# Optimization experiments

Measured on AMD Instinct MI355X. Metric: run time of the kernel, lower is better.

Reference implementation:

```python
import jax, jax.numpy as jnp
import numpy as np

N_NODES = 50000
N_EDGES = 800000
N_GRAPHS = 64
F_IN = 128
HID = 64
HEADS = 4
N_CLS = 10
NEG_SLOPE = 0.2


def _glorot(key, shape):
    fan_in, fan_out = shape[-1], shape[-2] if len(shape) > 1 else shape[-1]
    lim = jnp.sqrt(6.0 / (fan_in + fan_out))
    return jax.random.uniform(key, shape, jnp.float32, -lim, lim)


def setup_inputs() -> dict:
    key = jax.random.key(0)
    ks = jax.random.split(key, 20)
    x = jax.random.normal(ks[0], (N_NODES, F_IN), jnp.float32)
    edge_index = jax.random.randint(ks[1], (2, N_EDGES), 0, N_NODES, jnp.int32)
    batch = jnp.sort(jax.random.randint(ks[2], (N_NODES,), 0, N_GRAPHS, jnp.int32))
    HC = HID * HEADS
    return {
        "x": x, "edge_index": edge_index, "batch": batch,
        # node embedding Linear(F_IN -> HID)
        "W_emb": _glorot(ks[3], (HID, F_IN)), "b_emb": jnp.zeros((HID,), jnp.float32),
        # gat1: HID -> HID, heads=4, concat
        "W1": _glorot(ks[4], (HC, HID)),
        "a_src1": _glorot(ks[5], (HEADS, HID)), "a_dst1": _glorot(ks[6], (HEADS, HID)),
        "b1": jnp.zeros((HC,), jnp.float32),
        # gat2: HC -> HID, heads=4, concat
        "W2": _glorot(ks[7], (HC, HC)),
        "a_src2": _glorot(ks[8], (HEADS, HID)), "a_dst2": _glorot(ks[9], (HEADS, HID)),
        "b2": jnp.zeros((HC,), jnp.float32),
        # gat3: HC -> HID, heads=1, mean
        "W3": _glorot(ks[10], (HID, HC)),
        "a_src3": _glorot(ks[11], (1, HID)), "a_dst3": _glorot(ks[12], (1, HID)),
        "b3": jnp.zeros((HID,), jnp.float32),
        # classifier: Linear(2*HID -> HID), ReLU, Linear(HID -> N_CLS)
        "Wc1": _glorot(ks[13], (HID, 2 * HID)), "bc1": jnp.zeros((HID,), jnp.float32),
        "Wc2": _glorot(ks[14], (N_CLS, HID)), "bc2": jnp.zeros((N_CLS,), jnp.float32),
    }


def _gat_layer(x, src, dst, W, a_src, a_dst, b, concat):
    """PyG-style GATConv (eval mode, self-loops already in src/dst)."""
    N = x.shape[0]
    H, C = a_src.shape
    h = (x @ W.T).reshape(N, H, C)                       # [N,H,C]
    s = jnp.einsum("nhc,hc->nh", h, a_src)               # [N,H]
    d = jnp.einsum("nhc,hc->nh", h, a_dst)               # [N,H]
    e = jax.nn.leaky_relu(s[src] + d[dst], NEG_SLOPE)    # [E,H]
    emax = jax.lax.stop_gradient(jax.ops.segment_max(e, dst, num_segments=N))
    emax = jnp.where(jnp.isfinite(emax), emax, 0.0)
    ex = jnp.exp(e - emax[dst])
    den = jax.ops.segment_sum(ex, dst, num_segments=N)   # [N,H]
    alpha = ex / (den[dst] + 1e-16)                      # segment softmax
    out = jax.ops.segment_sum(h[src] * alpha[:, :, None], dst, num_segments=N)
    out = out.reshape(N, H * C) if concat else out.mean(axis=1)
    return out + b


def reference(x, edge_index, batch, W_emb, b_emb, W1, a_src1, a_dst1, b1,
              W2, a_src2, a_dst2, b2, W3, a_src3, a_dst3, b3, Wc1, bc1, Wc2, bc2):
    N = x.shape[0]
    loops = jnp.arange(N, dtype=edge_index.dtype)
    src = jnp.concatenate([edge_index[0], loops])
    dst = jnp.concatenate([edge_index[1], loops])

    h = x @ W_emb.T + b_emb
    h = jax.nn.elu(_gat_layer(h, src, dst, W1, a_src1, a_dst1, b1, True))
    h = jax.nn.elu(_gat_layer(h, src, dst, W2, a_src2, a_dst2, b2, True))
    h = jax.nn.elu(_gat_layer(h, src, dst, W3, a_src3, a_dst3, b3, False))

    counts = jax.ops.segment_sum(jnp.ones((N,), h.dtype), batch, num_segments=N_GRAPHS)
    mean = jax.ops.segment_sum(h, batch, num_segments=N_GRAPHS) / jnp.maximum(counts, 1.0)[:, None]
    mx = jax.ops.segment_max(h, batch, num_segments=N_GRAPHS)
    mx = jnp.where(counts[:, None] > 0, mx, 0.0)
    g = jnp.concatenate([mean, mx], axis=1)              # [B, 2*HID]

    g = jax.nn.relu(g @ Wc1.T + bc1)
    return g @ Wc2.T + bc2                               # [B, N_CLS]
```

## Files before the change

kernel.cpp:

```cpp
#include <hip/hip_runtime.h>
#include <math.h>

#define NG 64
#define F_IN 128
#define NEG_SLOPE 0.2f

typedef __attribute__((ext_vector_type(8))) short s16x8;
typedef __attribute__((ext_vector_type(4))) float f32x4;

static __device__ __forceinline__ float elu_f(float x) { return x > 0.f ? x : expm1f(x); }
static __device__ __forceinline__ float lrelu(float x) { return x > 0.f ? x : NEG_SLOPE * x; }
static __device__ __forceinline__ unsigned enc_f32(float x) {
    unsigned u = __float_as_uint(x);
    return (u & 0x80000000u) ? ~u : (u | 0x80000000u);
}
static __device__ __forceinline__ float dec_f32(unsigned u) {
    unsigned b = (u & 0x80000000u) ? (u & 0x7fffffffu) : ~u;
    return __uint_as_float(b);
}
static __device__ __forceinline__ unsigned short bf16_rn(float x) {
    unsigned u = __float_as_uint(x);
    unsigned r = u + 0x7FFFu + ((u >> 16) & 1u);
    return (unsigned short)(r >> 16);
}
static __device__ __forceinline__ float bf16_to_f32(unsigned short h) {
    return __uint_as_float(((unsigned)h) << 16);
}

static __device__ __forceinline__ size_t fragaddr(int row, int k, int K) {
    return ((size_t)(row >> 4) * (K >> 5) + (k >> 5)) * 512
         + (size_t)(((k & 31) >> 3) * 128 + (row & 15) * 8 + (k & 7));
}

static __device__ __forceinline__ void frag_store8(const float* v, unsigned short* hi,
                                                   unsigned short* lo, int row, int k0, int K) {
    unsigned short h[8], l[8];
    #pragma unroll
    for (int i = 0; i < 8; ++i) {
        h[i] = bf16_rn(v[i]);
        l[i] = bf16_rn(v[i] - bf16_to_f32(h[i]));
    }
    size_t a = fragaddr(row, k0, K);
    *(ushort4*)&hi[a]     = make_ushort4(h[0], h[1], h[2], h[3]);
    *(ushort4*)&hi[a + 4] = make_ushort4(h[4], h[5], h[6], h[7]);
    *(ushort4*)&lo[a]     = make_ushort4(l[0], l[1], l[2], l[3]);
    *(ushort4*)&lo[a + 4] = make_ushort4(l[4], l[5], l[6], l[7]);
}

__global__ void convert_frag(const float* __restrict__ in, unsigned short* __restrict__ hi,
                             unsigned short* __restrict__ lo, int R, int K) {
    int t = blockIdx.x * blockDim.x + threadIdx.x;
    if (t * 8 >= R * K) return;
    int row = (t * 8) / K;
    int k0 = (t * 8) % K;
    float4 v0 = *(const float4*)&in[(size_t)row * K + k0];
    float4 v1 = *(const float4*)&in[(size_t)row * K + k0 + 4];
    float v[8] = {v0.x, v0.y, v0.z, v0.w, v1.x, v1.y, v1.z, v1.w};
    frag_store8(v, hi, lo, row, k0, K);
}

__global__ void convert_weights(const float* __restrict__ We, const float* __restrict__ W1,
                                const float* __restrict__ W2, const float* __restrict__ W3,
                                unsigned short* WhE, unsigned short* WlE,
                                unsigned short* Wh1, unsigned short* Wl1,
                                unsigned short* Wh2, unsigned short* Wl2,
                                unsigned short* Wh3, unsigned short* Wl3) {
    int b = blockIdx.x;
    const float* in; unsigned short* hi; unsigned short* lo; int R, K, base;
    if (b < 4)       { in = We; hi = WhE; lo = WlE; R = 64;  K = 128; base = 0; }
    else if (b < 12) { in = W1; hi = Wh1; lo = Wl1; R = 256; K = 64;  base = 4; }
    else if (b < 44) { in = W2; hi = Wh2; lo = Wl2; R = 256; K = 256; base = 12; }
    else             { in = W3; hi = Wh3; lo = Wl3; R = 64;  K = 256; base = 44; }
    int t = (b - base) * 256 + threadIdx.x;
    if (t * 8 >= R * K) return;
    int row = (t * 8) / K;
    int k0 = (t * 8) % K;
    float4 v0 = *(const float4*)&in[(size_t)row * K + k0];
    float4 v1 = *(const float4*)&in[(size_t)row * K + k0 + 4];
    float v[8] = {v0.x, v0.y, v0.z, v0.w, v1.x, v1.y, v1.z, v1.w};
    frag_store8(v, hi, lo, row, k0, K);
}

__global__ void uvec_kernel(const float* __restrict__ W1, const float* __restrict__ a1s,
                            const float* __restrict__ a1d,
                            float* __restrict__ us, float* __restrict__ ud) {
    int h = threadIdx.x >> 6;
    int i = threadIdx.x & 63;
    float s = 0.f, d = 0.f;
    for (int o = 0; o < 64; ++o) {
        float w = W1[(h * 64 + o) * 64 + i];
        s = fmaf(w, a1s[h * 64 + o], s);
        d = fmaf(w, a1d[h * 64 + o], d);
    }
    us[h * 64 + i] = s;
    ud[h * 64 + i] = d;
}

__global__ void hist_kernel(const int* __restrict__ ei, int* __restrict__ cnt, int E, int N) {
    int e = blockIdx.x * blockDim.x + threadIdx.x;
    int ET = E + N;
    if (e >= ET) return;
    int dst = (e < E) ? ei[E + e] : (e - E);
    atomicAdd(&cnt[dst], 1);
}

__global__ void scan1_kernel(const int* __restrict__ cnt, int* __restrict__ excl,
                             int* __restrict__ bsum, int n) {
    __shared__ int sm[256];
    int t = threadIdx.x;
    int base = blockIdx.x * 1024 + t * 4;
    int v[4];
    #pragma unroll
    for (int u = 0; u < 4; ++u) { int idx = base + u; v[u] = (idx < n) ? cnt[idx] : 0; }
    int tsum = v[0] + v[1] + v[2] + v[3];
    sm[t] = tsum;
    __syncthreads();
    for (int off = 1; off < 256; off <<= 1) {
        int y = (t >= off) ? sm[t - off] : 0;
        __syncthreads();
        sm[t] += y;
        __syncthreads();
    }
    int run = sm[t] - tsum;
    #pragma unroll
    for (int u = 0; u < 4; ++u) {
        int idx = base + u;
        if (idx < n) excl[idx] = run;
        run += v[u];
    }
    if (t == 255) bsum[blockIdx.x] = sm[255];
}

__global__ void scan2_kernel(int* __restrict__ bsum, int* __restrict__ offs, int nb, int n) {
    if (blockIdx.x == 0 && threadIdx.x == 0) {
        int run = 0;
        for (int b = 0; b < nb; ++b) { int t = bsum[b]; bsum[b] = run; run += t; }
        offs[n] = run;
    }
}

__global__ void scan3_kernel(int* __restrict__ offs, const int* __restrict__ bsum,
                             int* __restrict__ cur, int n) {
    int base = blockIdx.x * 1024 + threadIdx.x * 4;
    int add = bsum[blockIdx.x];
    #pragma unroll
    for (int u = 0; u < 4; ++u) {
        int idx = base + u;
        if (idx < n) { int v = offs[idx] + add; offs[idx] = v; cur[idx] = v; }
    }
}

__global__ void scatter_kernel(const int* __restrict__ ei, int* __restrict__ cur,
                               int* __restrict__ csr_src, int E, int N) {
    int e = blockIdx.x * blockDim.x + threadIdx.x;
    int ET = E + N;
    if (e >= ET) return;
    int src, dst;
    if (e < E) { src = ei[e]; dst = ei[E + e]; }
    else       { src = e - E; dst = e - E; }
    int pos = atomicAdd(&cur[dst], 1);
    csr_src[pos] = src;
}

template<int K, int AK, int BN, int HATT, bool SHARED, bool SLICED, bool DO_ELU, int OUTM>
__global__ __launch_bounds__(256) void gemm_frag(const unsigned short* __restrict__ Ahi,
                                                 const unsigned short* __restrict__ Alo,
                                                 const unsigned short* __restrict__ Whi,
                                                 const unsigned short* __restrict__ Wlo,
                                                 void* __restrict__ OutV,
                                                 unsigned short* __restrict__ Ohi,
                                                 unsigned short* __restrict__ Olo,
                                                 int M,
                                                 const float* __restrict__ bias,
                                                 const float* __restrict__ asrc,
                                                 const float* __restrict__ adst,
                                                 float* __restrict__ S, float* __restrict__ D,
                                                 int N) {
    constexpr int RF = (BN == 256) ? 4 : 2;
    const int t = threadIdx.x;
    const int lane = t & 63;
    const int w = t >> 6;
    const int lj = lane & 15;
    const int kg = lane >> 4;
    const int n0 = blockIdx.x * ((BN == 256) ? 64 : 128);
    const int m0 = blockIdx.y * BN;
    const int rbase = (BN == 256) ? 0 : w * 32;
    const int cbase = (BN == 256) ? w * 64 : 0;
    const int aoff = SLICED ? blockIdx.y * K : 0;
    const unsigned short* __restrict__ WhiB = SLICED ? Whi + (size_t)blockIdx.y * BN * K : Whi;
    const unsigned short* __restrict__ WloB = SLICED ? Wlo + (size_t)blockIdx.y * BN * K : Wlo;

    f32x4 acc[RF][4];
    #pragma unroll
    for (int rf = 0; rf < RF; ++rf)
        #pragma unroll
        for (int cf = 0; cf < 4; ++cf) acc[rf][cf] = (f32x4){0.f, 0.f, 0.f, 0.f};

    for (int kc = 0; kc < K; kc += 32) {
        s16x8 ah[RF], al[RF];
        #pragma unroll
        for (int rf = 0; rf < RF; ++rf) {
            size_t a = fragaddr(n0 + rbase + rf * 16 + lj, aoff + kc + kg * 8, AK);
            ah[rf] = *(const s16x8*)&Ahi[a];
            al[rf] = *(const s16x8*)&Alo[a];
        }
        #pragma unroll
        for (int cf = 0; cf < 4; ++cf) {
            int bcol = (SLICED ? 0 : m0) + cbase + cf * 16 + lj;
            size_t b = fragaddr(bcol, kc + kg * 8, K);
            s16x8 bh = *(const s16x8*)&WhiB[b];
            s16x8 bl = *(const s16x8*)&WloB[b];
            #pragma unroll
            for (int rf = 0; rf < RF; ++rf) {
                acc[rf][cf] = __builtin_amdgcn_mfma_f32_16x16x32_bf16(ah[rf], bh, acc[rf][cf], 0, 0, 0);
                acc[rf][cf] = __builtin_amdgcn_mfma_f32_16x16x32_bf16(ah[rf], bl, acc[rf][cf], 0, 0, 0);
                acc[rf][cf] = __builtin_amdgcn_mfma_f32_16x16x32_bf16(al[rf], bh, acc[rf][cf], 0, 0, 0);
            }
        }
    }

    #pragma unroll
    for (int cf = 0; cf < 4; ++cf) {
        int gcol = m0 + cbase + cf * 16 + lj;
        float bv = bias ? bias[gcol] : 0.f;
        #pragma unroll
        for (int rf = 0; rf < RF; ++rf) {
            #pragma unroll
            for (int r = 0; r < 4; ++r) {
                int gn = n0 + rbase + rf * 16 + (lane >> 4) * 4 + r;
                if (gn < N) {
                    float o = acc[rf][cf][r] + bv;
                    if (DO_ELU) o = elu_f(o);
                    if (OUTM == 0) {
                        ((float*)OutV)[(size_t)gn * M + gcol] = o;
                    } else if (OUTM == 1) {
                        ((unsigned short*)OutV)[(size_t)gn * M + gcol] = bf16_rn(o);
                    } else {
                        unsigned short hv = bf16_rn(o);
                        unsigned short lv = bf16_rn(o - bf16_to_f32(hv));
                        size_t a2 = fragaddr(gn, gcol, M);
                        Ohi[a2] = hv; Olo[a2] = lv;
                    }
                }
            }
        }
    }
    if (HATT > 0) {
        const int HS = SHARED ? HATT : 1;
        #pragma unroll
        for (int hh = 0; hh < HS; ++hh) {
            const int head = SHARED ? hh : w;
            float aw[4], dw[4], bw[4];
            #pragma unroll
            for (int c2 = 0; c2 < 4; ++c2) {
                aw[c2] = asrc[head * 64 + c2 * 16 + lj];
                dw[c2] = adst[head * 64 + c2 * 16 + lj];
                bw[c2] = bias ? bias[m0 + cbase + c2 * 16 + lj] : 0.f;
            }
            #pragma unroll
            for (int rf = 0; rf < RF; ++rf) {
                #pragma unroll
                for (int r = 0; r < 4; ++r) {
                    float sp = 0.f, dp = 0.f;
                    #pragma unroll
                    for (int c2 = 0; c2 < 4; ++c2) {
                        float vv = acc[rf][c2][r] + bw[c2];
                        sp = fmaf(vv, aw[c2], sp);
                        dp = fmaf(vv, dw[c2], dp);
                    }
                    #pragma unroll
                    for (int off = 1; off < 16; off <<= 1) {
                        sp += __shfl_xor(sp, off);
                        dp += __shfl_xor(dp, off);
                    }
                    if (lj == 0) {
                        int gn = n0 + rbase + rf * 16 + (lane >> 4) * 4 + r;
                        if (gn < N) { S[gn * HATT + head] = sp; D[gn * HATT + head] = dp; }
                    }
                }
            }
        }
    }
}

__global__ __launch_bounds__(256, 8) void gat_agg_x(const unsigned short* __restrict__ xb,
                                                    const float* __restrict__ s,
                                                    const float* __restrict__ d,
                                                    const int* __restrict__ offs,
                                                    const int* __restrict__ csr_src,
                                                    unsigned short* __restrict__ Gh,
                                                    unsigned short* __restrict__ Gl,
                                                    int N) {
    __shared__ float stash[4][64 * 5];
    int wv = threadIdx.x >> 6;
    int lane = threadIdx.x & 63;
    int node = (blockIdx.x * blockDim.x + threadIdx.x) >> 6;
    if (node >= N) return;
    float* st = stash[wv];
    int e0 = offs[node], e1 = offs[node + 1];
    float4 dv4 = *(const float4*)&d[node * 4];
    float dd[4] = {dv4.x, dv4.y, dv4.z, dv4.w};
    float mrun[4] = {-INFINITY, -INFINITY, -INFINITY, -INFINITY};
    float den[4] = {0.f, 0.f, 0.f, 0.f};
    float acc[4] = {0.f, 0.f, 0.f, 0.f};

    for (int base = e0; base < e1; base += 64) {
        int cnt = min(64, e1 - base);
        float ev[4] = {-INFINITY, -INFINITY, -INFINITY, -INFINITY};
        if (lane < cnt) {
            int src = csr_src[base + lane];
            float4 sv = *(const float4*)&s[src * 4];
            ev[0] = lrelu(sv.x + dd[0]); ev[1] = lrelu(sv.y + dd[1]);
            ev[2] = lrelu(sv.z + dd[2]); ev[3] = lrelu(sv.w + dd[3]);
            st[lane * 5 + 0] = ev[0]; st[lane * 5 + 1] = ev[1];
            st[lane * 5 + 2] = ev[2]; st[lane * 5 + 3] = ev[3];
            st[lane * 5 + 4] = __int_as_float(src);
        }
        #pragma unroll
        for (int h = 0; h < 4; ++h) {
            float m = ev[h];
            #pragma unroll
            for (int off = 32; off; off >>= 1) m = fmaxf(m, __shfl_xor(m, off));
            float mnew = fmaxf(mrun[h], m);
            float scale = __expf(mrun[h] - mnew);
            acc[h] *= scale; den[h] *= scale;
            mrun[h] = mnew;
        }
        int k = 0;
        for (; k + 4 <= cnt; k += 4) {
            int si[4];
            #pragma unroll
            for (int u = 0; u < 4; ++u) si[u] = __float_as_int(st[(k + u) * 5 + 4]);
            float vx[4];
            #pragma unroll
            for (int u = 0; u < 4; ++u) vx[u] = bf16_to_f32(xb[(size_t)si[u] * 64 + lane]);
            #pragma unroll
            for (int u = 0; u < 4; ++u) {
                #pragma unroll
                for (int h = 0; h < 4; ++h) {
                    float p = __expf(st[(k + u) * 5 + h] - mrun[h]);
                    den[h] += p;
                    acc[h] = fmaf(p, vx[u], acc[h]);
                }
            }
        }
        for (; k < cnt; ++k) {
            int src = __float_as_int(st[k * 5 + 4]);
            float v = bf16_to_f32(xb[(size_t)src * 64 + lane]);
            #pragma unroll
            for (int h = 0; h < 4; ++h) {
                float p = __expf(st[k * 5 + h] - mrun[h]);
                den[h] += p;
                acc[h] = fmaf(p, v, acc[h]);
            }
        }
    }
    #pragma unroll
    for (int h = 0; h < 4; ++h) {
        float v = acc[h] / (den[h] + 1e-16f);
        unsigned short hv = bf16_rn(v);
        unsigned short lv = bf16_rn(v - bf16_to_f32(hv));
        size_t a = fragaddr(node, h * 64 + lane, 256);
        Gh[a] = hv; Gl[a] = lv;
    }
}

template<bool FRAGOUT>
__global__ __launch_bounds__(256, 8) void gat_agg4(const unsigned short* __restrict__ hp,
                                                   const float* __restrict__ s,
                                                   const float* __restrict__ d,
                                                   const int* __restrict__ offs,
                                                   const int* __restrict__ csr_src,
                                                   const float* __restrict__ bias,
                                                   float* __restrict__ outF,
                                                   unsigned short* __restrict__ outHi,
                                                   unsigned short* __restrict__ outLo,
                                                   int N) {
    __shared__ float stash[4][64 * 5];
    int wv = threadIdx.x >> 6;
    int lane = threadIdx.x & 63;
    int node = (blockIdx.x * blockDim.x + threadIdx.x) >> 6;
    if (node >= N) return;
    float* st = stash[wv];
    int e0 = offs[node], e1 = offs[node + 1];

    float4 dv4 = *(const float4*)&d[node * 4];
    float dd[4] = {dv4.x, dv4.y, dv4.z, dv4.w};
    const int hd = lane >> 4;

    float mrun = -INFINITY;
    float acc0 = 0.f, acc1 = 0.f, acc2 = 0.f, acc3 = 0.f, den = 0.f;

    for (int base = e0; base < e1; base += 64) {
        int cnt = min(64, e1 - base);
        float ev[4] = {-INFINITY, -INFINITY, -INFINITY, -INFINITY};
        if (lane < cnt) {
            int src = csr_src[base + lane];
            float4 sv = *(const float4*)&s[src * 4];
            ev[0] = lrelu(sv.x + dd[0]); ev[1] = lrelu(sv.y + dd[1]);
            ev[2] = lrelu(sv.z + dd[2]); ev[3] = lrelu(sv.w + dd[3]);
            st[lane * 5 + 0] = ev[0]; st[lane * 5 + 1] = ev[1];
            st[lane * 5 + 2] = ev[2]; st[lane * 5 + 3] = ev[3];
            st[lane * 5 + 4] = __int_as_float(src);
        }
        float mc[4];
        #pragma unroll
        for (int h = 0; h < 4; ++h) {
            float m = ev[h];
            #pragma unroll
            for (int off = 32; off; off >>= 1) m = fmaxf(m, __shfl_xor(m, off));
            mc[h] = m;
        }
        float mch = (lane & 32) ? ((lane & 16) ? mc[3] : mc[2]) : ((lane & 16) ? mc[1] : mc[0]);
        float mnew = fmaxf(mrun, mch);
        float scale = __expf(mrun - mnew);
        acc0 *= scale; acc1 *= scale; acc2 *= scale; acc3 *= scale; den *= scale;
        mrun = mnew;

        int k = 0;
        for (; k + 4 <= cnt; k += 4) {
            float ea = st[(k + 0) * 5 + hd];
            float eb = st[(k + 1) * 5 + hd];
            float ec = st[(k + 2) * 5 + hd];
            float ed = st[(k + 3) * 5 + hd];
            int sa = __float_as_int(st[(k + 0) * 5 + 4]);
            int sb = __float_as_int(st[(k + 1) * 5 + 4]);
            int sc = __float_as_int(st[(k + 2) * 5 + 4]);
            int sd_ = __float_as_int(st[(k + 3) * 5 + 4]);
            float pa = __expf(ea - mrun);
            float pb = __expf(eb - mrun);
            float pc = __expf(ec - mrun);
            float pd = __expf(ed - mrun);
            den += (pa + pb) + (pc + pd);
            uint2 ua = *(const uint2*)&hp[(size_t)sa * 256 + lane * 4];
            uint2 ub = *(const uint2*)&hp[(size_t)sb * 256 + lane * 4];
            uint2 uc = *(const uint2*)&hp[(size_t)sc * 256 + lane * 4];
            uint2 ud = *(const uint2*)&hp[(size_t)sd_ * 256 + lane * 4];
            acc0 = fmaf(pa, __uint_as_float((ua.x & 0xffffu) << 16), acc0);
            acc1 = fmaf(pa, __uint_as_float(ua.x & 0xffff0000u), acc1);
            acc2 = fmaf(pa, __uint_as_float((ua.y & 0xffffu) << 16), acc2);
            acc3 = fmaf(pa, __uint_as_float(ua.y & 0xffff0000u), acc3);
            acc0 = fmaf(pb, __uint_as_float((ub.x & 0xffffu) << 16), acc0);
            acc1 = fmaf(pb, __uint_as_float(ub.x & 0xffff0000u), acc1);
            acc2 = fmaf(pb, __uint_as_float((ub.y & 0xffffu) << 16), acc2);
            acc3 = fmaf(pb, __uint_as_float(ub.y & 0xffff0000u), acc3);
            acc0 = fmaf(pc, __uint_as_float((uc.x & 0xffffu) << 16), acc0);
            acc1 = fmaf(pc, __uint_as_float(uc.x & 0xffff0000u), acc1);
            acc2 = fmaf(pc, __uint_as_float((uc.y & 0xffffu) << 16), acc2);
            acc3 = fmaf(pc, __uint_as_float(uc.y & 0xffff0000u), acc3);
            acc0 = fmaf(pd, __uint_as_float((ud.x & 0xffffu) << 16), acc0);
            acc1 = fmaf(pd, __uint_as_float(ud.x & 0xffff0000u), acc1);
            acc2 = fmaf(pd, __uint_as_float((ud.y & 0xffffu) << 16), acc2);
            acc3 = fmaf(pd, __uint_as_float(ud.y & 0xffff0000u), acc3);
        }
        for (; k < cnt; ++k) {
            float e = st[k * 5 + hd];
            int src = __float_as_int(st[k * 5 + 4]);
            float p = __expf(e - mrun);
            den += p;
            uint2 uv = *(const uint2*)&hp[(size_t)src * 256 + lane * 4];
            acc0 = fmaf(p, __uint_as_float((uv.x & 0xffffu) << 16), acc0);
            acc1 = fmaf(p, __uint_as_float(uv.x & 0xffff0000u), acc1);
            acc2 = fmaf(p, __uint_as_float((uv.y & 0xffffu) << 16), acc2);
            acc3 = fmaf(p, __uint_as_float(uv.y & 0xffff0000u), acc3);
        }
    }

    float inv = 1.0f / (den + 1e-16f);
    float4 bv = *(const float4*)&bias[lane * 4];
    float o0 = elu_f(acc0 * inv + bv.x);
    float o1 = elu_f(acc1 * inv + bv.y);
    float o2 = elu_f(acc2 * inv + bv.z);
    float o3 = elu_f(acc3 * inv + bv.w);
    if (FRAGOUT) {
        unsigned short h0 = bf16_rn(o0), h1 = bf16_rn(o1), h2 = bf16_rn(o2), h3 = bf16_rn(o3);
        ushort4 hq = make_ushort4(h0, h1, h2, h3);
        ushort4 lq = make_ushort4(bf16_rn(o0 - bf16_to_f32(h0)),
                                  bf16_rn(o1 - bf16_to_f32(h1)),
                                  bf16_rn(o2 - bf16_to_f32(h2)),
                                  bf16_rn(o3 - bf16_to_f32(h3)));
        size_t a = fragaddr(node, lane * 4, 256);
        *(ushort4*)&outHi[a] = hq;
        *(ushort4*)&outLo[a] = lq;
    } else {
        float4 o = make_float4(o0, o1, o2, o3);
        *(float4*)&outF[(size_t)node * 256 + lane * 4] = o;
    }
}

__global__ __launch_bounds__(256, 8) void gat_agg1(const unsigned short* __restrict__ hp,
                                                   const float* __restrict__ s,
                                                   const float* __restrict__ d,
                                                   const int* __restrict__ offs,
                                                   const int* __restrict__ csr_src,
                                                   const float* __restrict__ bias,
                                                   float* __restrict__ outF, int N) {
    __shared__ float stash[4][64 * 2];
    int wv = threadIdx.x >> 6;
    int lane = threadIdx.x & 63;
    int node = (blockIdx.x * blockDim.x + threadIdx.x) >> 6;
    if (node >= N) return;
    float* st = stash[wv];
    int e0 = offs[node], e1 = offs[node + 1];
    float dd = d[node];

    float mrun = -INFINITY;
    float acc0 = 0.f, den = 0.f;

    for (int base = e0; base < e1; base += 64) {
        int cnt = min(64, e1 - base);
        float ev = -INFINITY;
        if (lane < cnt) {
            int src = csr_src[base + lane];
            ev = lrelu(s[src] + dd);
            st[lane * 2 + 0] = ev;
            st[lane * 2 + 1] = __int_as_float(src);
        }
        float m = ev;
        #pragma unroll
        for (int off = 32; off; off >>= 1) m = fmaxf(m, __shfl_xor(m, off));
        float mnew = fmaxf(mrun, m);
        float scale = __expf(mrun - mnew);
        acc0 *= scale; den *= scale;
        mrun = mnew;

        int k = 0;
        for (; k + 4 <= cnt; k += 4) {
            float ea = st[(k + 0) * 2];
            float eb = st[(k + 1) * 2];
            float ec = st[(k + 2) * 2];
            float ed = st[(k + 3) * 2];
            int sa = __float_as_int(st[(k + 0) * 2 + 1]);
            int sb = __float_as_int(st[(k + 1) * 2 + 1]);
            int sc = __float_as_int(st[(k + 2) * 2 + 1]);
            int sd_ = __float_as_int(st[(k + 3) * 2 + 1]);
            float pa = __expf(ea - mrun);
            float pb = __expf(eb - mrun);
            float pc = __expf(ec - mrun);
            float pd = __expf(ed - mrun);
            den += (pa + pb) + (pc + pd);
            float ha = bf16_to_f32(hp[(size_t)sa * 64 + lane]);
            float hb = bf16_to_f32(hp[(size_t)sb * 64 + lane]);
            float hc = bf16_to_f32(hp[(size_t)sc * 64 + lane]);
            float hdv = bf16_to_f32(hp[(size_t)sd_ * 64 + lane]);
            acc0 = fmaf(pa, ha, acc0);
            acc0 = fmaf(pb, hb, acc0);
            acc0 = fmaf(pc, hc, acc0);
            acc0 = fmaf(pd, hdv, acc0);
        }
        for (; k < cnt; ++k) {
            float e = st[k * 2];
            int src = __float_as_int(st[k * 2 + 1]);
            float p = __expf(e - mrun);
            den += p;
            acc0 = fmaf(p, bf16_to_f32(hp[(size_t)src * 64 + lane]), acc0);
        }
    }
    float inv = 1.0f / (den + 1e-16f);
    outF[(size_t)node * 64 + lane] = elu_f(acc0 * inv + bias[lane]);
}

__global__ void pool_init(float* gsum, unsigned* gmax, int* gcnt) {
    int t = blockIdx.x * blockDim.x + threadIdx.x;
    if (t < NG * 64) { gsum[t] = 0.f; gmax[t] = enc_f32(-INFINITY); }
    if (t < NG) gcnt[t] = 0;
}

__global__ void pool_reduce(const float* __restrict__ h3, const int* __restrict__ batch,
                            float* __restrict__ gsum, unsigned* __restrict__ gmax,
                            int* __restrict__ gcnt, int N, int per) {
    int w = (blockIdx.x * blockDim.x + threadIdx.x) >> 6;
    int lane = threadIdx.x & 63;
    int n0 = w * per;
    int n1 = min(N, n0 + per);
    float lsum = 0.f, lmax = -INFINITY;
    int cur = -1, cnt = 0;
    for (int n = n0; n < n1; ++n) {
        int g = batch[n];
        if (g != cur) {
            if (cur >= 0) {
                atomicAdd(&gsum[cur * 64 + lane], lsum);
                atomicMax(&gmax[cur * 64 + lane], enc_f32(lmax));
                if (lane == 0) atomicAdd(&gcnt[cur], cnt);
            }
            cur = g; lsum = 0.f; lmax = -INFINITY; cnt = 0;
        }
        float v = h3[(size_t)n * 64 + lane];
        lsum += v; lmax = fmaxf(lmax, v); cnt++;
    }
    if (cur >= 0) {
        atomicAdd(&gsum[cur * 64 + lane], lsum);
        atomicMax(&gmax[cur * 64 + lane], enc_f32(lmax));
        if (lane == 0) atomicAdd(&gcnt[cur], cnt);
    }
}

__global__ __launch_bounds__(128) void classifier(const float* __restrict__ gsum,
                                                  const unsigned* __restrict__ gmax,
                                                  const int* __restrict__ gcnt,
                                                  const float* __restrict__ Wc1,
                                                  const float* __restrict__ bc1,
                                                  const float* __restrict__ Wc2,
                                                  const float* __restrict__ bc2,
                                                  float* __restrict__ out) {
    __shared__ float gv[128];
    __shared__ float z1[64];
    int g = blockIdx.x, t = threadIdx.x;
    int cnt = gcnt[g];
    if (t < 64) {
        gv[t] = gsum[g * 64 + t] / fmaxf((float)cnt, 1.f);
    } else {
        float mx = dec_f32(gmax[g * 64 + (t - 64)]);
        gv[t] = (cnt > 0) ? mx : 0.f;
    }
    __syncthreads();
    if (t < 64) {
        float a = bc1[t];
        for (int k = 0; k < 128; ++k) a = fmaf(Wc1[t * 128 + k], gv[k], a);
        z1[t] = a > 0.f ? a : 0.f;
    }
    __syncthreads();
    if (t < 10) {
        float a = bc2[t];
        for (int k = 0; k < 64; ++k) a = fmaf(Wc2[t * 64 + k], z1[k], a);
        out[g * 10 + t] = a;
    }
}

extern "C" void kernel_launch(void* const* d_in, const int* in_sizes, int n_in,
                              void* d_out, int out_size, void* d_ws, size_t ws_size,
                              hipStream_t stream) {
    const float* x      = (const float*)d_in[0];
    const int*   ei     = (const int*)d_in[1];
    const int*   batch  = (const int*)d_in[2];
    const float* W_emb  = (const float*)d_in[3];
    const float* b_emb  = (const float*)d_in[4];
    const float* W1     = (const float*)d_in[5];
    const float* as1    = (const float*)d_in[6];
    const float* ad1    = (const float*)d_in[7];
    const float* b1     = (const float*)d_in[8];
    const float* W2     = (const float*)d_in[9];
    const float* as2    = (const float*)d_in[10];
    const float* ad2    = (const float*)d_in[11];
    const float* b2     = (const float*)d_in[12];
    const float* W3     = (const float*)d_in[13];
    const float* as3    = (const float*)d_in[14];
    const float* ad3    = (const float*)d_in[15];
    const float* b3     = (const float*)d_in[16];
    const float* Wc1    = (const float*)d_in[17];
    const float* bc1    = (const float*)d_in[18];
    const float* Wc2    = (const float*)d_in[19];
    const float* bc2    = (const float*)d_in[20];

    const int N = in_sizes[0] / F_IN;
    const int E = in_sizes[1] / 2;
    const int ET = E + N;
    const int GB64 = (N + 63) / 64;
    const int GB128 = (N + 127) / 128;
    const int ROWS_FR = ((N + 255) / 256) * 256;
    const size_t FR128 = (size_t)(ROWS_FR / 16) * (128 / 32) * 512;
    const size_t FR256 = (size_t)(ROWS_FR / 16) * (256 / 32) * 512;

    size_t off = 0;
    auto alloc = [&](size_t bytes) -> void* {
        void* p = (char*)d_ws + off;
        off += (bytes + 255) & ~(size_t)255;
        return p;
    };
    unsigned short* Xh  = (unsigned short*)alloc(FR128 * 2);
    unsigned short* Xl  = (unsigned short*)alloc(FR128 * 2);
    unsigned short* Aemb= (unsigned short*)alloc((size_t)N * 64 * 2);
    unsigned short* Gh  = (unsigned short*)alloc(FR256 * 2);
    unsigned short* Gl  = (unsigned short*)alloc(FR256 * 2);
    unsigned short* C1h = (unsigned short*)alloc(FR256 * 2);
    unsigned short* C1l = (unsigned short*)alloc(FR256 * 2);
    unsigned short* H2b = (unsigned short*)alloc((size_t)N * 256 * 2);
    unsigned short* WhE = (unsigned short*)alloc(64 * 128 * 2);
    unsigned short* WlE = (unsigned short*)alloc(64 * 128 * 2);
    unsigned short* Wh1 = (unsigned short*)alloc(256 * 64 * 2);
    unsigned short* Wl1 = (unsigned short*)alloc(256 * 64 * 2);
    unsigned short* Wh2 = (unsigned short*)alloc(256 * 256 * 2);
    unsigned short* Wl2 = (unsigned short*)alloc(256 * 256 * 2);
    unsigned short* Wh3 = (unsigned short*)alloc(64 * 256 * 2);
    unsigned short* Wl3 = (unsigned short*)alloc(64 * 256 * 2);
    float*    us1     = (float*)alloc(4 * 64 * 4);
    float*    ud1     = (float*)alloc(4 * 64 * 4);
    float*    S       = (float*)alloc((size_t)N * 4 * 4);
    float*    D       = (float*)alloc((size_t)N * 4 * 4);
    int*      offs    = (int*)alloc((size_t)(N + 1) * 4);
    int*      cnt     = (int*)alloc((size_t)N * 4);
    int*      bsum    = (int*)alloc(64 * 4);
    int*      csr_src = (int*)alloc((size_t)ET * 4);
    float*    gsum    = (float*)alloc(NG * 64 * 4);
    unsigned* gmax    = (unsigned*)alloc(NG * 64 * 4);
    int*      gcnt    = (int*)alloc(NG * 4);
    (void)ws_size; (void)n_in; (void)out_size;

    const int SCB = (N + 1023) / 1024;

    convert_frag<<<(N * 128 / 8 + 255) / 256, 256, 0, stream>>>(x, Xh, Xl, N, 128);
    convert_weights<<<52, 256, 0, stream>>>(W_emb, W1, W2, W3, WhE, WlE, Wh1, Wl1,
                                            Wh2, Wl2, Wh3, Wl3);
    uvec_kernel<<<1, 256, 0, stream>>>(W1, as1, ad1, us1, ud1);

    hipMemsetAsync(cnt, 0, (size_t)N * 4, stream);
    hist_kernel<<<(ET + 255) / 256, 256, 0, stream>>>(ei, cnt, E, N);
    scan1_kernel<<<SCB, 256, 0, stream>>>(cnt, offs, bsum, N);
    scan2_kernel<<<1, 64, 0, stream>>>(bsum, offs, SCB, N);
    scan3_kernel<<<SCB, 256, 0, stream>>>(offs, bsum, cnt, N);
    scatter_kernel<<<(ET + 255) / 256, 256, 0, stream>>>(ei, cnt, csr_src, E, N);

    const int NWV = (N * 64 + 255) / 256;

    gemm_frag<128, 128, 64, 4, true, false, false, 1><<<dim3(GB128, 1), 256, 0, stream>>>(
        Xh, Xl, WhE, WlE, Aemb, nullptr, nullptr, 64, b_emb, us1, ud1, S, D, N);
    gat_agg_x<<<NWV, 256, 0, stream>>>(Aemb, S, D, offs, csr_src, Gh, Gl, N);
    gemm_frag<64, 256, 64, 0, false, true, true, 3><<<dim3(GB128, 4), 256, 0, stream>>>(
        Gh, Gl, Wh1, Wl1, nullptr, C1h, C1l, 256, b1, nullptr, nullptr, nullptr, nullptr, N);
    gemm_frag<256, 256, 256, 4, false, false, false, 1><<<dim3(GB64, 1), 256, 0, stream>>>(
        C1h, C1l, Wh2, Wl2, H2b, nullptr, nullptr, 256, nullptr, as2, ad2, S, D, N);
    gat_agg4<true><<<NWV, 256, 0, stream>>>(H2b, S, D, offs, csr_src, b2,
                                            nullptr, Gh, Gl, N);
    gemm_frag<256, 256, 64, 1, true, false, false, 1><<<dim3(GB128, 1), 256, 0, stream>>>(
        Gh, Gl, Wh3, Wl3, Aemb, nullptr, nullptr, 64, nullptr, as3, ad3, S, D, N);
    gat_agg1<<<NWV, 256, 0, stream>>>(Aemb, S, D, offs, csr_src, b3, (float*)H2b, N);

    pool_init<<<16, 256, 0, stream>>>(gsum, gmax, gcnt);
    const int PBLK = 512;
    int per = (N + PBLK * 4 - 1) / (PBLK * 4);
    pool_reduce<<<PBLK, 256, 0, stream>>>((const float*)H2b, batch, gsum, gmax, gcnt, N, per);
    classifier<<<NG, 128, 0, stream>>>(gsum, gmax, gcnt, Wc1, bc1, Wc2, bc2, (float*)d_out);
}
```

Measured before the change: 539.2 us.

## Replace online softmax with a global per-head max bound computed in the GEMM epilogue

The GEMM epilogue now reduces the per-head maximum of the source attention scores into a global atomic value. The aggregation kernels use lrelu(max_s + d) as a fixed upper bound on each node's edge logits. This removes the per-chunk wave max reductions and accumulator rescaling of the online softmax, and exponentials are computed once per edge when stashed rather than per lane per use. The risk is underflow: if a node's logits sit far below the global bound, all its weights could round to zero. The epsilon guard on the denominator was also removed, so that case would divide by zero.

Measured after the change: 631.9 us. 17.2% more time.

```diff
diff --git a/kernel.cpp b/kernel.cpp
--- a/kernel.cpp
+++ b/kernel.cpp
@@ -175,6 +175,7 @@
                                                  const float* __restrict__ asrc,
                                                  const float* __restrict__ adst,
                                                  float* __restrict__ S, float* __restrict__ D,
+                                                 unsigned* __restrict__ smaxE,
                                                  int N) {
     constexpr int RF = (BN == 256) ? 4 : 2;
     const int t = threadIdx.x;
@@ -247,6 +248,9 @@
     }
     if (HATT > 0) {
         const int HS = SHARED ? HATT : 1;
+        float lsmax[HS];
+        #pragma unroll
+        for (int hh = 0; hh < HS; ++hh) lsmax[hh] = -INFINITY;
         #pragma unroll
         for (int hh = 0; hh < HS; ++hh) {
             const int head = SHARED ? hh : w;
@@ -273,6 +277,7 @@
                         sp += __shfl_xor(sp, off);
                         dp += __shfl_xor(dp, off);
                     }
+                    lsmax[hh] = fmaxf(lsmax[hh], sp);
                     if (lj == 0) {
                         int gn = n0 + rbase + rf * 16 + (lane >> 4) * 4 + r;
                         if (gn < N) { S[gn * HATT + head] = sp; D[gn * HATT + head] = dp; }
@@ -280,6 +285,13 @@
                 }
             }
         }
+        #pragma unroll
+        for (int hh = 0; hh < HS; ++hh) {
+            float m = lsmax[hh];
+            #pragma unroll
+            for (int off = 32; off; off >>= 1) m = fmaxf(m, __shfl_xor(m, off));
+            if (lane == 0) atomicMax(&smaxE[SHARED ? hh : w], enc_f32(m));
+        }
     }
 }
 
@@ -288,6 +300,7 @@
                                                     const float* __restrict__ d,
                                                     const int* __restrict__ offs,
                                                     const int* __restrict__ csr_src,
+                                                    const unsigned* __restrict__ smaxE,
                                                     unsigned short* __restrict__ Gh,
                                                     unsigned short* __restrict__ Gl,
                                                     int N) {
@@ -300,31 +313,22 @@
     int e0 = offs[node], e1 = offs[node + 1];
     float4 dv4 = *(const float4*)&d[node * 4];
     float dd[4] = {dv4.x, dv4.y, dv4.z, dv4.w};
-    float mrun[4] = {-INFINITY, -INFINITY, -INFINITY, -INFINITY};
+    float mh[4];
+    #pragma unroll
+    for (int h = 0; h < 4; ++h) mh[h] = lrelu(dec_f32(smaxE[h]) + dd[h]);
     float den[4] = {0.f, 0.f, 0.f, 0.f};
     float acc[4] = {0.f, 0.f, 0.f, 0.f};
 
     for (int base = e0; base < e1; base += 64) {
         int cnt = min(64, e1 - base);
-        float ev[4] = {-INFINITY, -INFINITY, -INFINITY, -INFINITY};
         if (lane < cnt) {
             int src = csr_src[base + lane];
             float4 sv = *(const float4*)&s[src * 4];
-            ev[0] = lrelu(sv.x + dd[0]); ev[1] = lrelu(sv.y + dd[1]);
-            ev[2] = lrelu(sv.z + dd[2]); ev[3] = lrelu(sv.w + dd[3]);
-            st[lane * 5 + 0] = ev[0]; st[lane * 5 + 1] = ev[1];
-            st[lane * 5 + 2] = ev[2]; st[lane * 5 + 3] = ev[3];
+            st[lane * 5 + 0] = __expf(lrelu(sv.x + dd[0]) - mh[0]);
+            st[lane * 5 + 1] = __expf(lrelu(sv.y + dd[1]) - mh[1]);
+            st[lane * 5 + 2] = __expf(lrelu(sv.z + dd[2]) - mh[2]);
+            st[lane * 5 + 3] = __expf(lrelu(sv.w + dd[3]) - mh[3]);
             st[lane * 5 + 4] = __int_as_float(src);
-        }
-        #pragma unroll
-        for (int h = 0; h < 4; ++h) {
-            float m = ev[h];
-            #pragma unroll
-            for (int off = 32; off; off >>= 1) m = fmaxf(m, __shfl_xor(m, off));
-            float mnew = fmaxf(mrun[h], m);
-            float scale = __expf(mrun[h] - mnew);
-            acc[h] *= scale; den[h] *= scale;
-            mrun[h] = mnew;
         }
         int k = 0;
         for (; k + 4 <= cnt; k += 4) {
@@ -338,7 +342,7 @@
             for (int u = 0; u < 4; ++u) {
                 #pragma unroll
                 for (int h = 0; h < 4; ++h) {
-                    float p = __expf(st[(k + u) * 5 + h] - mrun[h]);
+                    float p = st[(k + u) * 5 + h];
                     den[h] += p;
                     acc[h] = fmaf(p, vx[u], acc[h]);
                 }
@@ -349,7 +353,7 @@
             float v = bf16_to_f32(xb[(size_t)src * 64 + lane]);
             #pragma unroll
             for (int h = 0; h < 4; ++h) {
-                float p = __expf(st[k * 5 + h] - mrun[h]);
+                float p = st[k * 5 + h];
                 den[h] += p;
                 acc[h] = fmaf(p, v, acc[h]);
             }
@@ -357,7 +361,7 @@
     }
     #pragma unroll
     for (int h = 0; h < 4; ++h) {
-        float v = acc[h] / (den[h] + 1e-16f);
+        float v = acc[h] / den[h];
         unsigned short hv = bf16_rn(v);
         unsigned short lv = bf16_rn(v - bf16_to_f32(hv));
         size_t a = fragaddr(node, h * 64 + lane, 256);
@@ -371,6 +375,7 @@
                                                    const float* __restrict__ d,
                                                    const int* __restrict__ offs,
                                                    const int* __restrict__ csr_src,
+                                                   const unsigned* __restrict__ smaxE,
                                                    const float* __restrict__ bias,
                                                    float* __restrict__ outF,
                                                    unsigned short* __restrict__ outHi,
@@ -386,51 +391,34 @@
 
     float4 dv4 = *(const float4*)&d[node * 4];
     float dd[4] = {dv4.x, dv4.y, dv4.z, dv4.w};
+    float mh[4];
+    #pragma unroll
+    for (int h = 0; h < 4; ++h) mh[h] = lrelu(dec_f32(smaxE[h]) + dd[h]);
     const int hd = lane >> 4;
 
-    float mrun = -INFINITY;
     float acc0 = 0.f, acc1 = 0.f, acc2 = 0.f, acc3 = 0.f, den = 0.f;
 
     for (int base = e0; base < e1; base += 64) {
         int cnt = min(64, e1 - base);
-        float ev[4] = {-INFINITY, -INFINITY, -INFINITY, -INFINITY};
         if (lane < cnt) {
             int src = csr_src[base + lane];
             float4 sv = *(const float4*)&s[src * 4];
-            ev[0] = lrelu(sv.x + dd[0]); ev[1] = lrelu(sv.y + dd[1]);
-            ev[2] = lrelu(sv.z + dd[2]); ev[3] = lrelu(sv.w + dd[3]);
-            st[lane * 5 + 0] = ev[0]; st[lane * 5 + 1] = ev[1];
-            st[lane * 5 + 2] = ev[2]; st[lane * 5 + 3] = ev[3];
+            st[lane * 5 + 0] = __expf(lrelu(sv.x + dd[0]) - mh[0]);
+            st[lane * 5 + 1] = __expf(lrelu(sv.y + dd[1]) - mh[1]);
+            st[lane * 5 + 2] = __expf(lrelu(sv.z + dd[2]) - mh[2]);
+            st[lane * 5 + 3] = __expf(lrelu(sv.w + dd[3]) - mh[3]);
             st[lane * 5 + 4] = __int_as_float(src);
         }
-        float mc[4];
-        #pragma unroll
-        for (int h = 0; h < 4; ++h) {
-            float m = ev[h];
-            #pragma unroll
-            for (int off = 32; off; off >>= 1) m = fmaxf(m, __shfl_xor(m, off));
-            mc[h] = m;
-        }
-        float mch = (lane & 32) ? ((lane & 16) ? mc[3] : mc[2]) : ((lane & 16) ? mc[1] : mc[0]);
-        float mnew = fmaxf(mrun, mch);
-        float scale = __expf(mrun - mnew);
-        acc0 *= scale; acc1 *= scale; acc2 *= scale; acc3 *= scale; den *= scale;
-        mrun = mnew;
-
         int k = 0;
         for (; k + 4 <= cnt; k += 4) {
-            float ea = st[(k + 0) * 5 + hd];
-            float eb = st[(k + 1) * 5 + hd];
-            float ec = st[(k + 2) * 5 + hd];
-            float ed = st[(k + 3) * 5 + hd];
+            float pa = st[(k + 0) * 5 + hd];
+            float pb = st[(k + 1) * 5 + hd];
+            float pc = st[(k + 2) * 5 + hd];
+            float pd = st[(k + 3) * 5 + hd];
             int sa = __float_as_int(st[(k + 0) * 5 + 4]);
             int sb = __float_as_int(st[(k + 1) * 5 + 4]);
             int sc = __float_as_int(st[(k + 2) * 5 + 4]);
             int sd_ = __float_as_int(st[(k + 3) * 5 + 4]);
-            float pa = __expf(ea - mrun);
-            float pb = __expf(eb - mrun);
-            float pc = __expf(ec - mrun);
-            float pd = __expf(ed - mrun);
             den += (pa + pb) + (pc + pd);
             uint2 ua = *(const uint2*)&hp[(size_t)sa * 256 + lane * 4];
             uint2 ub = *(const uint2*)&hp[(size_t)sb * 256 + lane * 4];
@@ -454,9 +442,8 @@
             acc3 = fmaf(pd, __uint_as_float(ud.y & 0xffff0000u), acc3);
         }
         for (; k < cnt; ++k) {
-            float e = st[k * 5 + hd];
+            float p = st[k * 5 + hd];
             int src = __float_as_int(st[k * 5 + 4]);
-            float p = __expf(e - mrun);
             den += p;
             uint2 uv = *(const uint2*)&hp[(size_t)src * 256 + lane * 4];
             acc0 = fmaf(p, __uint_as_float((uv.x & 0xffffu) << 16), acc0);
@@ -466,7 +453,7 @@
         }
     }
 
-    float inv = 1.0f / (den + 1e-16f);
+    float inv = 1.0f / den;
     float4 bv = *(const float4*)&bias[lane * 4];
     float o0 = elu_f(acc0 * inv + bv.x);
     float o1 = elu_f(acc1 * inv + bv.y);
@@ -493,6 +480,7 @@
                                                    const float* __restrict__ d,
                                                    const int* __restrict__ offs,
                                                    const int* __restrict__ csr_src,
+                                                   const unsigned* __restrict__ smaxE,
                                                    const float* __restrict__ bias,
                                                    float* __restrict__ outF, int N) {
     __shared__ float stash[4][64 * 2];
@@ -503,41 +491,27 @@
     float* st = stash[wv];
     int e0 = offs[node], e1 = offs[node + 1];
     float dd = d[node];
-
-    float mrun = -INFINITY;
+    float mh = lrelu(dec_f32(smaxE[0]) + dd);
+
     float acc0 = 0.f, den = 0.f;
 
     for (int base = e0; base < e1; base += 64) {
         int cnt = min(64, e1 - base);
-        float ev = -INFINITY;
         if (lane < cnt) {
             int src = csr_src[base + lane];
-            ev = lrelu(s[src] + dd);
-            st[lane * 2 + 0] = ev;
+            st[lane * 2 + 0] = __expf(lrelu(s[src] + dd) - mh);
             st[lane * 2 + 1] = __int_as_float(src);
         }
-        float m = ev;
-        #pragma unroll
-        for (int off = 32; off; off >>= 1) m = fmaxf(m, __shfl_xor(m, off));
-        float mnew = fmaxf(mrun, m);
-        float scale = __expf(mrun - mnew);
-        acc0 *= scale; den *= scale;
-        mrun = mnew;
-
         int k = 0;
         for (; k + 4 <= cnt; k += 4) {
-            float ea = st[(k + 0) * 2];
-            float eb = st[(k + 1) * 2];
-            float ec = st[(k + 2) * 2];
-            float ed = st[(k + 3) * 2];
+            float pa = st[(k + 0) * 2];
+            float pb = st[(k + 1) * 2];
+            float pc = st[(k + 2) * 2];
+            float pd = st[(k + 3) * 2];
             int sa = __float_as_int(st[(k + 0) * 2 + 1]);
             int sb = __float_as_int(st[(k + 1) * 2 + 1]);
             int sc = __float_as_int(st[(k + 2) * 2 + 1]);
             int sd_ = __float_as_int(st[(k + 3) * 2 + 1]);
-            float pa = __expf(ea - mrun);
-            float pb = __expf(eb - mrun);
-            float pc = __expf(ec - mrun);
-            float pd = __expf(ed - mrun);
             den += (pa + pb) + (pc + pd);
             float ha = bf16_to_f32(hp[(size_t)sa * 64 + lane]);
             float hb = bf16_to_f32(hp[(size_t)sb * 64 + lane]);
@@ -549,21 +523,23 @@
             acc0 = fmaf(pd, hdv, acc0);
         }
         for (; k < cnt; ++k) {
-            float e = st[k * 2];
+            float p = st[k * 2];
             int src = __float_as_int(st[k * 2 + 1]);
-            float p = __expf(e - mrun);
             den += p;
             acc0 = fmaf(p, bf16_to_f32(hp[(size_t)src * 64 + lane]), acc0);
         }
     }
-    float inv = 1.0f / (den + 1e-16f);
-    outF[(size_t)node * 64 + lane] = elu_f(acc0 * inv + bias[lane]);
-}
-
-__global__ void pool_init(float* gsum, unsigned* gmax, int* gcnt) {
+    outF[(size_t)node * 64 + lane] = elu_f(acc0 / den + bias[lane]);
+}
+
+__global__ void pool_init(float* gsum, unsigned* gmax, int* gcnt,
+                          unsigned* smax1, unsigned* smax2, unsigned* smax3) {
     int t = blockIdx.x * blockDim.x + threadIdx.x;
-    if (t < NG * 64) { gsum[t] = 0.f; gmax[t] = enc_f32(-INFINITY); }
+    const unsigned NEGINF = 0x007FFFFFu;
+    if (t < NG * 64) { gsum[t] = 0.f; gmax[t] = NEGINF; }
     if (t < NG) gcnt[t] = 0;
+    if (t < 4) { smax1[t] = NEGINF; smax2[t] = NEGINF; }
+    if (t == 0) smax3[0] = NEGINF;
 }
 
 __global__ void pool_reduce(const float* __restrict__ h3, const int* __restrict__ batch,
@@ -687,6 +663,9 @@
     float*    ud1     = (float*)alloc(4 * 64 * 4);
     float*    S       = (float*)alloc((size_t)N * 4 * 4);
     float*    D       = (float*)alloc((size_t)N * 4 * 4);
+    unsigned* smax1   = (unsigned*)alloc(4 * 4);
+    unsigned* smax2   = (unsigned*)alloc(4 * 4);
+    unsigned* smax3   = (unsigned*)alloc(4 * 4);
     int*      offs    = (int*)alloc((size_t)(N + 1) * 4);
     int*      cnt     = (int*)alloc((size_t)N * 4);
     int*      bsum    = (int*)alloc(64 * 4);
@@ -698,6 +677,8 @@
 
     const int SCB = (N + 1023) / 1024;
 
+    pool_init<<<16, 256, 0, stream>>>(gsum, gmax, gcnt, smax1, smax2, smax3);
+
     convert_frag<<<(N * 128 / 8 + 255) / 256, 256, 0, stream>>>(x, Xh, Xl, N, 128);
     convert_weights<<<52, 256, 0, stream>>>(W_emb, W1, W2, W3, WhE, WlE, Wh1, Wl1,
                                             Wh2, Wl2, Wh3, Wl3);
@@ -713,19 +694,19 @@
     const int NWV = (N * 64 + 255) / 256;
 
     gemm_frag<128, 128, 64, 4, true, false, false, 1><<<dim3(GB128, 1), 256, 0, stream>>>(
-        Xh, Xl, WhE, WlE, Aemb, nullptr, nullptr, 64, b_emb, us1, ud1, S, D, N);
-    gat_agg_x<<<NWV, 256, 0, stream>>>(Aemb, S, D, offs, csr_src, Gh, Gl, N);
+        Xh, Xl, WhE, WlE, Aemb, nullptr, nullptr, 64, b_emb, us1, ud1, S, D, smax1, N);
+    gat_agg_x<<<NWV, 256, 0, stream>>>(Aemb, S, D, offs, csr_src, smax1, Gh, Gl, N);
     gemm_frag<64, 256, 64, 0, false, true, true, 3><<<dim3(GB128, 4), 256, 0, stream>>>(
-        Gh, Gl, Wh1, Wl1, nullptr, C1h, C1l, 256, b1, nullptr, nullptr, nullptr, nullptr, N);
+        Gh, Gl, Wh1, Wl1, nullptr, C1h, C1l, 256, b1, nullptr, nullptr, nullptr, nullptr,
+        nullptr, N);
     gemm_frag<256, 256, 256, 4, false, false, false, 1><<<dim3(GB64, 1), 256, 0, stream>>>(
-        C1h, C1l, Wh2, Wl2, H2b, nullptr, nullptr, 256, nullptr, as2, ad2, S, D, N);
-    gat_agg4<true><<<NWV, 256, 0, stream>>>(H2b, S, D, offs, csr_src, b2,
+        C1h, C1l, Wh2, Wl2, H2b, nullptr, nullptr, 256, nullptr, as2, ad2, S, D, smax2, N);
+    gat_agg4<true><<<NWV, 256, 0, stream>>>(H2b, S, D, offs, csr_src, smax2, b2,
                                             nullptr, Gh, Gl, N);
     gemm_frag<256, 256, 64, 1, true, false, false, 1><<<dim3(GB128, 1), 256, 0, stream>>>(
-        Gh, Gl, Wh3, Wl3, Aemb, nullptr, nullptr, 64, nullptr, as3, ad3, S, D, N);
-    gat_agg1<<<NWV, 256, 0, stream>>>(Aemb, S, D, offs, csr_src, b3, (float*)H2b, N);
-
-    pool_init<<<16, 256, 0, stream>>>(gsum, gmax, gcnt);
+        Gh, Gl, Wh3, Wl3, Aemb, nullptr, nullptr, 64, nullptr, as3, ad3, S, D, smax3, N);
+    gat_agg1<<<NWV, 256, 0, stream>>>(Aemb, S, D, offs, csr_src, smax3, b3, (float*)H2b, N);
+
     const int PBLK = 512;
     int per = (N + PBLK * 4 - 1) / (PBLK * 4);
     pool_reduce<<<PBLK, 256, 0, stream>>>((const float*)H2b, batch, gsum, gmax, gcnt, N, per);
```
